# Performance work log

Hardware: AMD Instinct MI355X
Metric: run time of the kernel (lower is better)

Reference implementation:

```python
import jax, jax.numpy as jnp
import numpy as np

B, F, H, C = 256, 512, 1024, 1000
LN_EPS = 1e-5


def _proj(x, W, b, g, be):
    # AdaptiveAvgPool2d(1) + Flatten + Linear + LayerNorm + GELU(exact)
    p = x.mean(axis=(2, 3))                       # [B, Cin]
    h = p @ W + b                                 # [B, F]
    mu = h.mean(axis=-1, keepdims=True)
    var = h.var(axis=-1, keepdims=True)           # ddof=0, matches torch LayerNorm
    h = (h - mu) / jnp.sqrt(var + LN_EPS) * g + be
    return jax.nn.gelu(h, approximate=False)


def setup_inputs() -> dict:
    key = jax.random.key(0)
    ks = iter(jax.random.split(key, 64))
    def rn(shape, s=1.0):
        return jax.random.normal(next(ks), shape, jnp.float32) * s
    inp = {}
    feats = {"s1": (16, 112), "s2": (24, 56), "s3": (40, 28), "s4": (80, 14), "s5": (160, 7)}
    for n, (c, hw) in feats.items():
        inp[n] = rn((B, c, hw, hw))
    inp["ff"] = rn((B, 960, 7, 7))
    for i, c in enumerate([16, 24, 40, 80, 160], start=1):
        inp[f"Wp{i}"] = rn((c, F), 0.02)
        inp[f"bp{i}"] = jnp.zeros((F,), jnp.float32)
        inp[f"g{i}"] = jnp.ones((F,), jnp.float32)
        inp[f"be{i}"] = jnp.zeros((F,), jnp.float32)
    inp["Wg1"] = rn((960, H), 0.02); inp["bg1"] = jnp.zeros((H,), jnp.float32)
    inp["Wg2"] = rn((H, H // 2), 0.02); inp["bg2"] = jnp.zeros((H // 2,), jnp.float32)
    inp["Wg3"] = rn((H // 2, 5), 0.02); inp["bg3"] = jnp.zeros((5,), jnp.float32)
    inp["Wc1"] = rn((F, H), 0.02); inp["bc1"] = jnp.zeros((H,), jnp.float32)
    inp["Wc2"] = rn((H, H // 2), 0.02); inp["bc2"] = jnp.zeros((H // 2,), jnp.float32)
    inp["Wc3"] = rn((H // 2, C), 0.02); inp["bc3"] = jnp.zeros((C,), jnp.float32)
    return inp


def reference(s1, s2, s3, s4, s5, ff,
              Wp1, bp1, g1, be1, Wp2, bp2, g2, be2, Wp3, bp3, g3, be3,
              Wp4, bp4, g4, be4, Wp5, bp5, g5, be5,
              Wg1, bg1, Wg2, bg2, Wg3, bg3,
              Wc1, bc1, Wc2, bc2, Wc3, bc3):
    # gate on pooled final backbone features (dropout inactive at eval)
    gate_in = ff.mean(axis=(2, 3))                         # [B, 960]
    h = jax.nn.relu(gate_in @ Wg1 + bg1)
    h = jax.nn.relu(h @ Wg2 + bg2)
    gate_logits = h @ Wg3 + bg3                            # [B, 5]

    # per-stage projections -> [B, 5, F]
    stack = jnp.stack([
        _proj(s1, Wp1, bp1, g1, be1),
        _proj(s2, Wp2, bp2, g2, be2),
        _proj(s3, Wp3, bp3, g3, be3),
        _proj(s4, Wp4, bp4, g4, be4),
        _proj(s5, Wp5, bp5, g5, be5),
    ], axis=1)

    topv, topi = jax.lax.top_k(gate_logits, 2)             # [B, 2]
    w = jax.nn.softmax(topv, axis=1)                       # softmax over top-k logits
    sel = jnp.take_along_axis(stack, topi[:, :, None], axis=1)  # [B, 2, F]
    mixture = (sel * w[:, :, None]).sum(axis=1)            # [B, F]

    h = jax.nn.relu(mixture @ Wc1 + bc1)
    h = jax.nn.relu(h @ Wc2 + bc2)
    logits = h @ Wc3 + bc3                                 # [B, C]
    return logits, gate_logits, topi, w
```

## Files before the change

### kernel.cpp

```cpp
#include <hip/hip_runtime.h>
#include <math.h>


typedef float nt4 __attribute__((ext_vector_type(4)));

__device__ __forceinline__ float4 ntload(const float4* p) {
    nt4 v = __builtin_nontemporal_load((const nt4*)p);
    return make_float4(v.x, v.y, v.z, v.w);
}

struct PoolAll {
    const float* src[4];
    float*       dst[4];
    int n4[4];
    int cum[4];
    float inv[4];
    const float* s5;
    const float* ff;
    float*       dst5;
    float*       dstf;
    int nbb;
    int rows5;
};

__global__ __launch_bounds__(256) void pool_all_kernel(PoolAll S) {
    __shared__ float lds[64 * 49];
    if ((int)blockIdx.x < S.nbb) {
        int gid  = blockIdx.x * 256 + threadIdx.x;
        int wave = gid >> 6;
        int lane = gid & 63;
        if (wave >= S.cum[3]) return;
        int s = 0;
        #pragma unroll
        for (int i = 0; i < 3; ++i) if (wave >= S.cum[i]) s = i + 1;
        int row = wave - (s == 0 ? 0 : S.cum[s - 1]);
        const int n4 = S.n4[s];
        const float4* p4 = (const float4*)(S.src[s]) + (size_t)row * n4;
        float a0 = 0.f, a1 = 0.f, a2 = 0.f, a3 = 0.f;
        float a4 = 0.f, a5 = 0.f, a6 = 0.f, a7 = 0.f;
        int k = lane;
        for (; k + 448 < n4; k += 512) {
            float4 v0 = ntload(p4 + k);       float4 v1 = ntload(p4 + k + 64);
            float4 v2 = ntload(p4 + k + 128); float4 v3 = ntload(p4 + k + 192);
            float4 v4 = ntload(p4 + k + 256); float4 v5 = ntload(p4 + k + 320);
            float4 v6 = ntload(p4 + k + 384); float4 v7 = ntload(p4 + k + 448);
            a0 += (v0.x + v0.y) + (v0.z + v0.w);
            a1 += (v1.x + v1.y) + (v1.z + v1.w);
            a2 += (v2.x + v2.y) + (v2.z + v2.w);
            a3 += (v3.x + v3.y) + (v3.z + v3.w);
            a4 += (v4.x + v4.y) + (v4.z + v4.w);
            a5 += (v5.x + v5.y) + (v5.z + v5.w);
            a6 += (v6.x + v6.y) + (v6.z + v6.w);
            a7 += (v7.x + v7.y) + (v7.z + v7.w);
        }
        for (; k + 192 < n4; k += 256) {
            float4 v0 = ntload(p4 + k);       float4 v1 = ntload(p4 + k + 64);
            float4 v2 = ntload(p4 + k + 128); float4 v3 = ntload(p4 + k + 192);
            a0 += (v0.x + v0.y) + (v0.z + v0.w);
            a1 += (v1.x + v1.y) + (v1.z + v1.w);
            a2 += (v2.x + v2.y) + (v2.z + v2.w);
            a3 += (v3.x + v3.y) + (v3.z + v3.w);
        }
        for (; k < n4; k += 64) {
            float4 v = ntload(p4 + k);
            a0 += (v.x + v.y) + (v.z + v.w);
        }
        float acc = ((a0 + a1) + (a2 + a3)) + ((a4 + a5) + (a6 + a7));
        #pragma unroll
        for (int off = 32; off > 0; off >>= 1) acc += __shfl_down(acc, off, 64);
        if (lane == 0) S.dst[s][row] = acc * S.inv[s];
        return;
    }
    const int tid  = threadIdx.x;
    const int row0 = (blockIdx.x - S.nbb) * 64;
    const float* src;
    float* dst;
    int rbase;
    if (row0 < S.rows5) { src = S.s5; dst = S.dst5; rbase = row0; }
    else                { src = S.ff; dst = S.dstf; rbase = row0 - S.rows5; }
    const float4* p4 = (const float4*)(src + (size_t)rbase * 49);
    float4* l4 = (float4*)lds;
    float4 v0 = ntload(p4 + tid);
    float4 v1 = ntload(p4 + tid + 256);
    float4 v2 = ntload(p4 + tid + 512);
    float4 v3;
    const bool t3 = (tid < 784 - 768);
    if (t3) v3 = ntload(p4 + tid + 768);
    l4[tid]       = v0;
    l4[tid + 256] = v1;
    l4[tid + 512] = v2;
    if (t3) l4[tid + 768] = v3;
    __syncthreads();
    const int r  = tid >> 2;
    const int c0 = tid & 3;
    float s = 0.f;
    #pragma unroll
    for (int c = c0; c < 49; c += 4) s += lds[r * 49 + c];
    s += __shfl_down(s, 2, 64);
    s += __shfl_down(s, 1, 64);
    if (c0 == 0) dst[rbase + r] = s * (1.f / 49.f);
}

__device__ void fc_tile_body(const float* __restrict__ X,
        const float* __restrict__ W, float* __restrict__ Pt,
        int M, int K, int N, int Kc, int ntiles, int bid,
        float (*Xs)[68], float (*Ws)[68]) {
    const int tpk = 4 * ntiles;
    int ks  = bid / tpk;
    int rem = bid - ks * tpk;
    int mt  = rem / ntiles;
    int nt  = rem - mt * ntiles;
    const int m0 = mt * 64, n0 = nt * 64;
    const int k0 = ks * Kc;
    int k1 = k0 + Kc; if (k1 > K) k1 = K;

    const int tid = threadIdx.x;
    const int tm = tid & 15;
    const int tn = tid >> 4;
    const int xr = tid >> 2, xc = tid & 3;
    const int wr = tid >> 4, wc = tid & 15;
    const int nwc = n0 + wc * 4;

    float4 acc[4];
    #pragma unroll
    for (int r = 0; r < 4; ++r) acc[r] = make_float4(0.f, 0.f, 0.f, 0.f);

    float4 xv, wv;
    xv = *(const float4*)(X + (size_t)(m0 + xr) * K + k0 + xc * 4);
    if (nwc + 3 < N) {
        wv = *(const float4*)(W + (size_t)(k0 + wr) * N + nwc);
    } else {
        wv.x = (nwc + 0 < N) ? W[(size_t)(k0 + wr) * N + nwc + 0] : 0.f;
        wv.y = (nwc + 1 < N) ? W[(size_t)(k0 + wr) * N + nwc + 1] : 0.f;
        wv.z = (nwc + 2 < N) ? W[(size_t)(k0 + wr) * N + nwc + 2] : 0.f;
        wv.w = (nwc + 3 < N) ? W[(size_t)(k0 + wr) * N + nwc + 3] : 0.f;
    }

    for (int kt = k0; kt < k1; kt += 16) {
        __syncthreads();
        Xs[xc * 4 + 0][xr] = xv.x;
        Xs[xc * 4 + 1][xr] = xv.y;
        Xs[xc * 4 + 2][xr] = xv.z;
        Xs[xc * 4 + 3][xr] = xv.w;
        *(float4*)&Ws[wr][wc * 4] = wv;
        __syncthreads();
        if (kt + 16 < k1) {
            xv = *(const float4*)(X + (size_t)(m0 + xr) * K + kt + 16 + xc * 4);
            if (nwc + 3 < N) {
                wv = *(const float4*)(W + (size_t)(kt + 16 + wr) * N + nwc);
            } else {
                wv.x = (nwc + 0 < N) ? W[(size_t)(kt + 16 + wr) * N + nwc + 0] : 0.f;
                wv.y = (nwc + 1 < N) ? W[(size_t)(kt + 16 + wr) * N + nwc + 1] : 0.f;
                wv.z = (nwc + 2 < N) ? W[(size_t)(kt + 16 + wr) * N + nwc + 2] : 0.f;
                wv.w = (nwc + 3 < N) ? W[(size_t)(kt + 16 + wr) * N + nwc + 3] : 0.f;
            }
        }
        #pragma unroll
        for (int kk = 0; kk < 16; ++kk) {
            float4 xr4 = *(const float4*)&Xs[kk][tm * 4];
            float4 wr4 = *(const float4*)&Ws[kk][tn * 4];
            acc[0].x += xr4.x * wr4.x; acc[0].y += xr4.x * wr4.y;
            acc[0].z += xr4.x * wr4.z; acc[0].w += xr4.x * wr4.w;
            acc[1].x += xr4.y * wr4.x; acc[1].y += xr4.y * wr4.y;
            acc[1].z += xr4.y * wr4.z; acc[1].w += xr4.y * wr4.w;
            acc[2].x += xr4.z * wr4.x; acc[2].y += xr4.z * wr4.y;
            acc[2].z += xr4.z * wr4.z; acc[2].w += xr4.z * wr4.w;
            acc[3].x += xr4.w * wr4.x; acc[3].y += xr4.w * wr4.y;
            acc[3].z += xr4.w * wr4.z; acc[3].w += xr4.w * wr4.w;
        }
    }
    const int nbase = n0 + tn * 4;
    #pragma unroll
    for (int r = 0; r < 4; ++r) {
        int row = m0 + tm * 4 + r;
        float* pp = Pt + ((size_t)ks * M + row) * N + nbase;
        if (nbase + 3 < N) {
            *(float4*)pp = acc[r];
        } else {
            float vv[4] = { acc[r].x, acc[r].y, acc[r].z, acc[r].w };
            for (int c = 0; c < 4; ++c) if (nbase + c < N) pp[c] = vv[c];
        }
    }
}

__global__ __launch_bounds__(256) void fc_tile_kernel(const float* __restrict__ X,
        const float* __restrict__ W, float* __restrict__ Pt,
        int M, int K, int N, int Kc, int ntiles) {
    __shared__ __align__(16) float Xs[16][68];
    __shared__ __align__(16) float Ws[16][68];
    fc_tile_body(X, W, Pt, M, K, N, Kc, ntiles, blockIdx.x, Xs, Ws);
}

__global__ __launch_bounds__(256) void reduce_bias_kernel(const float* __restrict__ P,
        const float* __restrict__ bias, float* __restrict__ Y,
        int MN, int N, int KS, int do_relu) {
    int i = (blockIdx.x * 256 + threadIdx.x) * 4;
    if (i >= MN) return;
    float4 a = *(const float4*)(P + i);
    for (int s = 1; s < KS; ++s) {
        float4 b = *(const float4*)(P + (size_t)s * MN + i);
        a.x += b.x; a.y += b.y; a.z += b.z; a.w += b.w;
    }
    int n = i - (i / N) * N;
    float4 bb = *(const float4*)(bias + n);
    a.x += bb.x; a.y += bb.y; a.z += bb.z; a.w += bb.w;
    if (do_relu) {
        a.x = fmaxf(a.x, 0.f); a.y = fmaxf(a.y, 0.f);
        a.z = fmaxf(a.z, 0.f); a.w = fmaxf(a.w, 0.f);
    }
    *(float4*)(Y + i) = a;
}

struct ProjParams {
    const float* W[5];
    const float* bp[5];
    const float* g[5];
    const float* be[5];
    int K[5];
    int poff[5];
};

__device__ void proj_body(const ProjParams& P, const float* __restrict__ pools,
        float* __restrict__ proj_out, int task,
        float (*Xs)[68], float (*Ws)[68]) {
    const int st  = task >> 5;
    const int bid = task & 31;
    const int K  = P.K[st];
    const float* X = pools + P.poff[st];
    const float* W = P.W[st];
    const int N = 512;
    int mt  = bid >> 3;
    int nt  = bid & 7;
    const int m0 = mt * 64, n0 = nt * 64;

    const int tid = threadIdx.x;
    const int tm = tid & 15;
    const int tn = tid >> 4;
    const int xa = tid >> 3, xb = tid & 7;
    const int wc = tid & 63, wb = tid >> 6;
    const int nw = n0 + wc;

    float4 acc[4];
    #pragma unroll
    for (int r = 0; r < 4; ++r) acc[r] = make_float4(0.f, 0.f, 0.f, 0.f);

    float x0, x1, w0v, w1v;
    x0  = X[(size_t)(m0 + xa) * K + xb];
    x1  = X[(size_t)(m0 + xa + 32) * K + xb];
    w0v = W[(size_t)wb * N + nw];
    w1v = W[(size_t)(wb + 4) * N + nw];

    for (int kt = 0; kt < K; kt += 8) {
        __syncthreads();
        Xs[xb][xa] = x0; Xs[xb][xa + 32] = x1;
        Ws[wb][wc] = w0v; Ws[wb + 4][wc] = w1v;
        __syncthreads();
        if (kt + 8 < K) {
            x0  = X[(size_t)(m0 + xa) * K + kt + 8 + xb];
            x1  = X[(size_t)(m0 + xa + 32) * K + kt + 8 + xb];
            w0v = W[(size_t)(kt + 8 + wb) * N + nw];
            w1v = W[(size_t)(kt + 8 + wb + 4) * N + nw];
        }
        #pragma unroll
        for (int kk = 0; kk < 8; ++kk) {
            float4 xr = *(const float4*)&Xs[kk][tm * 4];
            float4 wr = *(const float4*)&Ws[kk][tn * 4];
            acc[0].x += xr.x * wr.x; acc[0].y += xr.x * wr.y;
            acc[0].z += xr.x * wr.z; acc[0].w += xr.x * wr.w;
            acc[1].x += xr.y * wr.x; acc[1].y += xr.y * wr.y;
            acc[1].z += xr.y * wr.z; acc[1].w += xr.y * wr.w;
            acc[2].x += xr.z * wr.x; acc[2].y += xr.z * wr.y;
            acc[2].z += xr.z * wr.z; acc[2].w += xr.z * wr.w;
            acc[3].x += xr.w * wr.x; acc[3].y += xr.w * wr.y;
            acc[3].z += xr.w * wr.z; acc[3].w += xr.w * wr.w;
        }
    }
    const int nbase = n0 + tn * 4;
    float4 bb = *(const float4*)(P.bp[st] + nbase);
    float* op = proj_out + (size_t)st * 131072 + (size_t)(m0 + tm * 4) * N + nbase;
    #pragma unroll
    for (int r = 0; r < 4; ++r) {
        float4 v = acc[r];
        v.x += bb.x; v.y += bb.y; v.z += bb.z; v.w += bb.w;
        *(float4*)(op + (size_t)r * N) = v;
    }
}

__global__ __launch_bounds__(256) void gate1_proj_kernel(
        const float* __restrict__ gate_in, const float* __restrict__ Wg1,
        float* __restrict__ slab, ProjParams P,
        const float* __restrict__ pools, float* __restrict__ proj_out) {
    __shared__ __align__(16) float Xs[16][68];
    __shared__ __align__(16) float Ws[16][68];
    if (blockIdx.x < 512) {
        fc_tile_body(gate_in, Wg1, slab, 256, 960, 1024, 128, 16,
                     blockIdx.x, Xs, Ws);
    } else {
        proj_body(P, pools, proj_out, blockIdx.x - 512,
                  (float(*)[68])Xs, (float(*)[68])Ws);
    }
}

__global__ __launch_bounds__(256) void fc3_mixln_kernel(
        const float* __restrict__ Xg, const float* __restrict__ Wg3,
        const float* __restrict__ bg3, ProjParams P,
        const float* __restrict__ proj_out, float* __restrict__ mix,
        float* __restrict__ out_gl, float* __restrict__ out_topi,
        float* __restrict__ out_w) {
    const int b    = blockIdx.x;
    const int tid  = threadIdx.x;
    const int lane = tid & 63;
    const int wv   = tid >> 6;
    __shared__ float red[4][5];
    __shared__ int   s_i0, s_i1;
    __shared__ float s_w0, s_w1;
    __shared__ float redS[4], redQ[4];
    __shared__ float s_mu, s_rstd;

    {
        const float* x = Xg + (size_t)b * 512;
        float acc[5] = {0.f, 0.f, 0.f, 0.f, 0.f};
        for (int k = tid; k < 512; k += 256) {
            float xv = x[k];
            const float* wr = Wg3 + (size_t)k * 5;
            acc[0] += xv * wr[0]; acc[1] += xv * wr[1]; acc[2] += xv * wr[2];
            acc[3] += xv * wr[3]; acc[4] += xv * wr[4];
        }
        #pragma unroll
        for (int off = 32; off > 0; off >>= 1) {
            #pragma unroll
            for (int j = 0; j < 5; ++j) acc[j] += __shfl_down(acc[j], off, 64);
        }
        if (lane == 0) {
            #pragma unroll
            for (int j = 0; j < 5; ++j) red[wv][j] = acc[j];
        }
        __syncthreads();
        if (tid == 0) {
            float v[5];
            #pragma unroll
            for (int j = 0; j < 5; ++j)
                v[j] = ((red[0][j] + red[1][j]) + (red[2][j] + red[3][j])) + bg3[j];
            int i0 = 0;
            #pragma unroll
            for (int i = 1; i < 5; ++i) if (v[i] > v[i0]) i0 = i;
            int i1 = -1;
            #pragma unroll
            for (int i = 0; i < 5; ++i) {
                if (i == i0) continue;
                if (i1 < 0 || v[i] > v[i1]) i1 = i;
            }
            float e1 = __expf(v[i1] - v[i0]);
            float inv = 1.f / (1.f + e1);
            float w0 = inv, w1 = e1 * inv;
            s_i0 = i0; s_i1 = i1; s_w0 = w0; s_w1 = w1;
            #pragma unroll
            for (int j = 0; j < 5; ++j) out_gl[b * 5 + j] = v[j];
            out_topi[b * 2]     = (float)i0;
            out_topi[b * 2 + 1] = (float)i1;
            out_w[b * 2]     = w0;
            out_w[b * 2 + 1] = w1;
        }
    }
    __syncthreads();

    float a0 = 0.f, a1 = 0.f;
    const int i0 = s_i0, i1 = s_i1;
    const float w0 = s_w0, w1 = s_w1;
    for (int j = 0; j < 2; ++j) {
        __syncthreads();
        const int st = j ? i1 : i0;
        const float w = j ? w1 : w0;
        const float* pp = proj_out + (size_t)st * 131072 + (size_t)b * 512;
        float h0 = pp[tid];
        float h1 = pp[tid + 256];
        float s = h0 + h1, q = h0 * h0 + h1 * h1;
        #pragma unroll
        for (int off = 32; off > 0; off >>= 1) {
            s += __shfl_down(s, off, 64);
            q += __shfl_down(q, off, 64);
        }
        if (lane == 0) { redS[wv] = s; redQ[wv] = q; }
        __syncthreads();
        if (tid == 0) {
            float ts = (redS[0] + redS[1]) + (redS[2] + redS[3]);
            float tq = (redQ[0] + redQ[1]) + (redQ[2] + redQ[3]);
            float mu  = ts * (1.f / 512.f);
            float var = tq * (1.f / 512.f) - mu * mu;
            s_mu   = mu;
            s_rstd = rsqrtf(var + 1e-5f);
        }
        __syncthreads();
        float mu = s_mu, rstd = s_rstd;
        float x0 = (h0 - mu) * rstd * P.g[st][tid] + P.be[st][tid];
        float x1 = (h1 - mu) * rstd * P.g[st][tid + 256] + P.be[st][tid + 256];
        a0 += w * (0.5f * x0 * (1.f + erff(x0 * 0.70710678118654752f)));
        a1 += w * (0.5f * x1 * (1.f + erff(x1 * 0.70710678118654752f)));
    }
    mix[(size_t)b * 512 + tid]       = a0;
    mix[(size_t)b * 512 + tid + 256] = a1;
}

extern "C" void kernel_launch(void* const* d_in, const int* in_sizes, int n_in,
                              void* d_out, int out_size, void* d_ws, size_t ws_size,
                              hipStream_t stream) {
    const int B = 256;

    const float* s1 = (const float*)d_in[0];
    const float* s2 = (const float*)d_in[1];
    const float* s3 = (const float*)d_in[2];
    const float* s4 = (const float*)d_in[3];
    const float* s5 = (const float*)d_in[4];
    const float* ff = (const float*)d_in[5];
    const float *Wp[5], *bp[5], *g[5], *be[5];
    for (int i = 0; i < 5; ++i) {
        Wp[i] = (const float*)d_in[6 + 4 * i];
        bp[i] = (const float*)d_in[7 + 4 * i];
        g[i]  = (const float*)d_in[8 + 4 * i];
        be[i] = (const float*)d_in[9 + 4 * i];
    }
    const float* Wg1 = (const float*)d_in[26]; const float* bg1 = (const float*)d_in[27];
    const float* Wg2 = (const float*)d_in[28]; const float* bg2 = (const float*)d_in[29];
    const float* Wg3 = (const float*)d_in[30]; const float* bg3 = (const float*)d_in[31];
    const float* Wc1 = (const float*)d_in[32]; const float* bc1 = (const float*)d_in[33];
    const float* Wc2 = (const float*)d_in[34]; const float* bc2 = (const float*)d_in[35];
    const float* Wc3 = (const float*)d_in[36]; const float* bc3 = (const float*)d_in[37];

    float* ws = (float*)d_ws;
    const int Ks[5]   = {16, 24, 40, 80, 160};
    const int poff[5] = {0, 4096, 10240, 20480, 40960};
    float* pools    = ws;
    float* gate_in  = ws + 81920;
    float* g1h      = ws + 327680;
    float* g2h      = ws + 589824;
    float* mix      = ws + 720896;
    float* proj_out = ws + 851968;
    float* c1h      = ws + 1507328;
    float* c2h      = ws + 1769472;
    float* slab     = ws + 1900544;

    float* out      = (float*)d_out;
    float* out_gl   = out + 256000;
    float* out_topi = out + 257280;
    float* out_w    = out + 257792;

    {
        PoolAll S;
        const float* srcs[4] = { s1, s2, s3, s4 };
        const int rls[4]  = { 112 * 112, 56 * 56, 28 * 28, 14 * 14 };
        const int rows[4] = { B * 16, B * 24, B * 40, B * 80 };
        int cum = 0;
        for (int i = 0; i < 4; ++i) {
            S.src[i] = srcs[i]; S.dst[i] = pools + poff[i]; S.n4[i] = rls[i] / 4;
            cum += rows[i]; S.cum[i] = cum; S.inv[i] = 1.f / rls[i];
        }
        S.nbb   = (cum * 64) / 256;
        S.s5    = s5; S.ff = ff;
        S.dst5  = pools + poff[4]; S.dstf = gate_in;
        S.rows5 = B * 160;
        int small_blocks = (S.rows5 + B * 960) / 64;
        pool_all_kernel<<<S.nbb + small_blocks, 256, 0, stream>>>(S);
    }

    ProjParams P;
    for (int i = 0; i < 5; ++i) {
        P.W[i] = Wp[i]; P.bp[i] = bp[i]; P.g[i] = g[i]; P.be[i] = be[i];
        P.K[i] = Ks[i]; P.poff[i] = poff[i];
    }

    gate1_proj_kernel<<<512 + 160, 256, 0, stream>>>(gate_in, Wg1, slab,
                                                     P, pools, proj_out);
    reduce_bias_kernel<<<(256 * 1024 / 4 + 255) / 256, 256, 0, stream>>>(
        slab, bg1, g1h, 256 * 1024, 1024, 8, 1);

    fc_tile_kernel<<<16 * 4 * 8, 256, 0, stream>>>(g1h, Wg2, slab,
                                                   256, 1024, 512, 64, 8);
    reduce_bias_kernel<<<(256 * 512 / 4 + 255) / 256, 256, 0, stream>>>(
        slab, bg2, g2h, 256 * 512, 512, 16, 1);

    fc3_mixln_kernel<<<B, 256, 0, stream>>>(g2h, Wg3, bg3, P, proj_out, mix,
                                            out_gl, out_topi, out_w);

    fc_tile_kernel<<<8 * 4 * 16, 256, 0, stream>>>(mix, Wc1, slab,
                                                   256, 512, 1024, 64, 16);
    reduce_bias_kernel<<<(256 * 1024 / 4 + 255) / 256, 256, 0, stream>>>(
        slab, bc1, c1h, 256 * 1024, 1024, 8, 1);
    fc_tile_kernel<<<16 * 4 * 8, 256, 0, stream>>>(c1h, Wc2, slab,
                                                   256, 1024, 512, 64, 8);
    reduce_bias_kernel<<<(256 * 512 / 4 + 255) / 256, 256, 0, stream>>>(
        slab, bc2, c2h, 256 * 512, 512, 16, 1);
    fc_tile_kernel<<<8 * 4 * 16, 256, 0, stream>>>(c2h, Wc3, slab,
                                                   256, 512, 1000, 64, 16);
    reduce_bias_kernel<<<(256 * 1000 / 4 + 255) / 256, 256, 0, stream>>>(
        slab, bc3, out, 256 * 1000, 1000, 8, 0);
}
```

Measured before the change: 533.0 us.

## Fuse split-K reduction, bias and ReLU into the next GEMM's input load

Removes the separate reduce_bias kernels between the chained MLP layers. Each following GEMM (and the gate fc3 kernel) now sums the split-K partial slabs, adds the bias and applies ReLU while loading its X tile. The Wc2 GEMM's K-chunk size also changes so it produces 8 partials instead of 16. This saves kernel launches and intermediate writes, but each GEMM block now re-reads 8 or 16 partial slabs for its X tile, which multiplies X-side memory traffic.

```diff
diff --git a/kernel.cpp b/kernel.cpp
--- a/kernel.cpp
+++ b/kernel.cpp
@@ -101,10 +101,11 @@
     if (c0 == 0) dst[rbase + r] = s * (1.f / 49.f);
 }
 
+template <int XKS>
 __device__ void fc_tile_body(const float* __restrict__ X,
-        const float* __restrict__ W, float* __restrict__ Pt,
-        int M, int K, int N, int Kc, int ntiles, int bid,
-        float (*Xs)[68], float (*Ws)[68]) {
+        const float* __restrict__ xbias, const float* __restrict__ W,
+        float* __restrict__ Pt, int M, int K, int N, int Kc, int ntiles,
+        int bid, float (*Xs)[68], float (*Ws)[68]) {
     const int tpk = 4 * ntiles;
     int ks  = bid / tpk;
     int rem = bid - ks * tpk;
@@ -120,32 +121,58 @@
     const int xr = tid >> 2, xc = tid & 3;
     const int wr = tid >> 4, wc = tid & 15;
     const int nwc = n0 + wc * 4;
+    const size_t MK = (size_t)M * K;
+    const size_t xrow = (size_t)(m0 + xr) * K;
 
     float4 acc[4];
     #pragma unroll
     for (int r = 0; r < 4; ++r) acc[r] = make_float4(0.f, 0.f, 0.f, 0.f);
 
-    float4 xv, wv;
-    xv = *(const float4*)(X + (size_t)(m0 + xr) * K + k0 + xc * 4);
-    if (nwc + 3 < N) {
-        wv = *(const float4*)(W + (size_t)(k0 + wr) * N + nwc);
-    } else {
-        wv.x = (nwc + 0 < N) ? W[(size_t)(k0 + wr) * N + nwc + 0] : 0.f;
-        wv.y = (nwc + 1 < N) ? W[(size_t)(k0 + wr) * N + nwc + 1] : 0.f;
-        wv.z = (nwc + 2 < N) ? W[(size_t)(k0 + wr) * N + nwc + 2] : 0.f;
-        wv.w = (nwc + 3 < N) ? W[(size_t)(k0 + wr) * N + nwc + 3] : 0.f;
+    const int NXV = (XKS > 0) ? XKS : 1;
+    float4 xv[NXV];
+    float4 wv;
+
+    {
+        const size_t xo = xrow + k0 + xc * 4;
+        #pragma unroll
+        for (int ss = 0; ss < NXV; ++ss)
+            xv[ss] = *(const float4*)(X + (size_t)ss * MK + xo);
+        if (nwc + 3 < N) {
+            wv = *(const float4*)(W + (size_t)(k0 + wr) * N + nwc);
+        } else {
+            wv.x = (nwc + 0 < N) ? W[(size_t)(k0 + wr) * N + nwc + 0] : 0.f;
+            wv.y = (nwc + 1 < N) ? W[(size_t)(k0 + wr) * N + nwc + 1] : 0.f;
+            wv.z = (nwc + 2 < N) ? W[(size_t)(k0 + wr) * N + nwc + 2] : 0.f;
+            wv.w = (nwc + 3 < N) ? W[(size_t)(k0 + wr) * N + nwc + 3] : 0.f;
+        }
     }
 
     for (int kt = k0; kt < k1; kt += 16) {
         __syncthreads();
-        Xs[xc * 4 + 0][xr] = xv.x;
-        Xs[xc * 4 + 1][xr] = xv.y;
-        Xs[xc * 4 + 2][xr] = xv.z;
-        Xs[xc * 4 + 3][xr] = xv.w;
+        float4 xs = xv[0];
+        if (XKS > 0) {
+            #pragma unroll
+            for (int ss = 1; ss < NXV; ++ss) {
+                xs.x += xv[ss].x; xs.y += xv[ss].y;
+                xs.z += xv[ss].z; xs.w += xv[ss].w;
+            }
+            float4 xb = *(const float4*)(xbias + kt + xc * 4);
+            xs.x = fmaxf(xs.x + xb.x, 0.f);
+            xs.y = fmaxf(xs.y + xb.y, 0.f);
+            xs.z = fmaxf(xs.z + xb.z, 0.f);
+            xs.w = fmaxf(xs.w + xb.w, 0.f);
+        }
+        Xs[xc * 4 + 0][xr] = xs.x;
+        Xs[xc * 4 + 1][xr] = xs.y;
+        Xs[xc * 4 + 2][xr] = xs.z;
+        Xs[xc * 4 + 3][xr] = xs.w;
         *(float4*)&Ws[wr][wc * 4] = wv;
         __syncthreads();
         if (kt + 16 < k1) {
-            xv = *(const float4*)(X + (size_t)(m0 + xr) * K + kt + 16 + xc * 4);
+            const size_t xo = xrow + kt + 16 + xc * 4;
+            #pragma unroll
+            for (int ss = 0; ss < NXV; ++ss)
+                xv[ss] = *(const float4*)(X + (size_t)ss * MK + xo);
             if (nwc + 3 < N) {
                 wv = *(const float4*)(W + (size_t)(kt + 16 + wr) * N + nwc);
             } else {
@@ -183,12 +210,13 @@
     }
 }
 
+template <int XKS>
 __global__ __launch_bounds__(256) void fc_tile_kernel(const float* __restrict__ X,
-        const float* __restrict__ W, float* __restrict__ Pt,
-        int M, int K, int N, int Kc, int ntiles) {
+        const float* __restrict__ xbias, const float* __restrict__ W,
+        float* __restrict__ Pt, int M, int K, int N, int Kc, int ntiles) {
     __shared__ __align__(16) float Xs[16][68];
     __shared__ __align__(16) float Ws[16][68];
-    fc_tile_body(X, W, Pt, M, K, N, Kc, ntiles, blockIdx.x, Xs, Ws);
+    fc_tile_body<XKS>(X, xbias, W, Pt, M, K, N, Kc, ntiles, blockIdx.x, Xs, Ws);
 }
 
 __global__ __launch_bounds__(256) void reduce_bias_kernel(const float* __restrict__ P,
@@ -293,8 +321,8 @@
     __shared__ __align__(16) float Xs[16][68];
     __shared__ __align__(16) float Ws[16][68];
     if (blockIdx.x < 512) {
-        fc_tile_body(gate_in, Wg1, slab, 256, 960, 1024, 128, 16,
-                     blockIdx.x, Xs, Ws);
+        fc_tile_body<0>(gate_in, nullptr, Wg1, slab, 256, 960, 1024, 128, 16,
+                        blockIdx.x, Xs, Ws);
     } else {
         proj_body(P, pools, proj_out, blockIdx.x - 512,
                   (float(*)[68])Xs, (float(*)[68])Ws);
@@ -302,11 +330,11 @@
 }
 
 __global__ __launch_bounds__(256) void fc3_mixln_kernel(
-        const float* __restrict__ Xg, const float* __restrict__ Wg3,
-        const float* __restrict__ bg3, ProjParams P,
-        const float* __restrict__ proj_out, float* __restrict__ mix,
-        float* __restrict__ out_gl, float* __restrict__ out_topi,
-        float* __restrict__ out_w) {
+        const float* __restrict__ Xp, const float* __restrict__ bg2,
+        const float* __restrict__ Wg3, const float* __restrict__ bg3,
+        ProjParams P, const float* __restrict__ proj_out,
+        float* __restrict__ mix, float* __restrict__ out_gl,
+        float* __restrict__ out_topi, float* __restrict__ out_w) {
     const int b    = blockIdx.x;
     const int tid  = threadIdx.x;
     const int lane = tid & 63;
@@ -318,10 +346,14 @@
     __shared__ float s_mu, s_rstd;
 
     {
-        const float* x = Xg + (size_t)b * 512;
+        const size_t MK = (size_t)256 * 512;
         float acc[5] = {0.f, 0.f, 0.f, 0.f, 0.f};
         for (int k = tid; k < 512; k += 256) {
-            float xv = x[k];
+            float v = Xp[(size_t)b * 512 + k];
+            #pragma unroll
+            for (int s = 1; s < 16; ++s)
+                v += Xp[(size_t)s * MK + (size_t)b * 512 + k];
+            float xv = fmaxf(v + bg2[k], 0.f);
             const float* wr = Wg3 + (size_t)k * 5;
             acc[0] += xv * wr[0]; acc[1] += xv * wr[1]; acc[2] += xv * wr[2];
             acc[3] += xv * wr[3]; acc[4] += xv * wr[4];
@@ -431,13 +463,10 @@
     const int poff[5] = {0, 4096, 10240, 20480, 40960};
     float* pools    = ws;
     float* gate_in  = ws + 81920;
-    float* g1h      = ws + 327680;
-    float* g2h      = ws + 589824;
-    float* mix      = ws + 720896;
-    float* proj_out = ws + 851968;
-    float* c1h      = ws + 1507328;
-    float* c2h      = ws + 1769472;
-    float* slab     = ws + 1900544;
+    float* mix      = ws + 327680;
+    float* proj_out = ws + 458752;
+    float* slabA    = ws + 1114112;
+    float* slabB    = ws + 3211264;
 
     float* out      = (float*)d_out;
     float* out_gl   = out + 256000;
@@ -468,29 +497,18 @@
         P.K[i] = Ks[i]; P.poff[i] = poff[i];
     }
 
-    gate1_proj_kernel<<<512 + 160, 256, 0, stream>>>(gate_in, Wg1, slab,
+    gate1_proj_kernel<<<512 + 160, 256, 0, stream>>>(gate_in, Wg1, slabA,
                                                      P, pools, proj_out);
-    reduce_bias_kernel<<<(256 * 1024 / 4 + 255) / 256, 256, 0, stream>>>(
-        slab, bg1, g1h, 256 * 1024, 1024, 8, 1);
-
-    fc_tile_kernel<<<16 * 4 * 8, 256, 0, stream>>>(g1h, Wg2, slab,
-                                                   256, 1024, 512, 64, 8);
-    reduce_bias_kernel<<<(256 * 512 / 4 + 255) / 256, 256, 0, stream>>>(
-        slab, bg2, g2h, 256 * 512, 512, 16, 1);
-
-    fc3_mixln_kernel<<<B, 256, 0, stream>>>(g2h, Wg3, bg3, P, proj_out, mix,
-                                            out_gl, out_topi, out_w);
-
-    fc_tile_kernel<<<8 * 4 * 16, 256, 0, stream>>>(mix, Wc1, slab,
-                                                   256, 512, 1024, 64, 16);
-    reduce_bias_kernel<<<(256 * 1024 / 4 + 255) / 256, 256, 0, stream>>>(
-        slab, bc1, c1h, 256 * 1024, 1024, 8, 1);
-    fc_tile_kernel<<<16 * 4 * 8, 256, 0, stream>>>(c1h, Wc2, slab,
-                                                   256, 1024, 512, 64, 8);
-    reduce_bias_kernel<<<(256 * 512 / 4 + 255) / 256, 256, 0, stream>>>(
-        slab, bc2, c2h, 256 * 512, 512, 16, 1);
-    fc_tile_kernel<<<8 * 4 * 16, 256, 0, stream>>>(c2h, Wc3, slab,
-                                                   256, 512, 1000, 64, 16);
+    fc_tile_kernel<8><<<16 * 4 * 8, 256, 0, stream>>>(
+        slabA, bg1, Wg2, slabB, 256, 1024, 512, 64, 8);
+    fc3_mixln_kernel<<<B, 256, 0, stream>>>(slabB, bg2, Wg3, bg3, P, proj_out,
+                                            mix, out_gl, out_topi, out_w);
+    fc_tile_kernel<0><<<8 * 4 * 16, 256, 0, stream>>>(
+        mix, nullptr, Wc1, slabA, 256, 512, 1024, 64, 16);
+    fc_tile_kernel<8><<<8 * 4 * 8, 256, 0, stream>>>(
+        slabA, bc1, Wc2, slabB, 256, 1024, 512, 128, 8);
+    fc_tile_kernel<8><<<8 * 4 * 16, 256, 0, stream>>>(
+        slabB, bc2, Wc3, slabA, 256, 512, 1000, 64, 16);
     reduce_bias_kernel<<<(256 * 1000 / 4 + 255) / 256, 256, 0, stream>>>(
-        slab, bc3, out, 256 * 1000, 1000, 8, 0);
-}
+        slabA, bc3, out, 256 * 1000, 1000, 8, 0);
+}
```

After: 524.8 us (median of 2 runs). About the same (-1.5%).
